# Kernel tuning notes

Hardware: AMD Instinct MI355X
Metric: run time of the kernel (lower is better)

The kernel has to match this reference:

```python
import jax, jax.numpy as jnp
import numpy as np

A = 10      # number of areas of interest
NPA = 192   # neurons per area
C = 128     # n_channels_per_region
B, T = 32, 1024
N = A * NPA # 1920 total neurons


def setup_inputs() -> dict:
    key = jax.random.key(0)
    k1, k2, k3 = jax.random.split(key, 3)
    x = jax.random.normal(k1, (B, T, N), jnp.float32)
    # per-area linear weights, stored [A, n_in, n_out] (nn.Linear W.T), and biases
    W = jax.random.normal(k2, (A, NPA, C), jnp.float32) / np.sqrt(NPA)
    b = jax.random.normal(k3, (A, C), jnp.float32) * 0.01
    # area label per neuron, identical across batch (code uses neuron_regions[0]);
    # permute neuron order so the per-area gather is irregular
    labels = jnp.repeat(jnp.arange(A, dtype=jnp.int32), NPA)
    perm = jax.random.permutation(jax.random.key(7), N)
    labels = labels[perm]
    neuron_regions = jnp.tile(labels[None, :], (B, 1))
    is_left = jnp.zeros((B, N), dtype=bool)  # unused by forward body
    return {"x": x, "W": W, "b": b, "neuron_regions": neuron_regions, "is_left": is_left}


def reference(x, W, b, neuron_regions, is_left):
    # halfbin_X=0, smoothing=False -> preprocess_X is identity, repeat_interleave no-op
    nr = np.asarray(neuron_regions[0])                      # static per-session labels
    A_, n, C_ = W.shape
    # gather indices per area; equal counts per area -> rectangular [A, n]
    idx = np.stack([np.where(nr == a)[0] for a in range(A_)])
    x_area = x[:, :, idx]                                   # [B, T, A, n] gather
    emb = jnp.einsum('btan,anc->btac', x_area, W) + b       # per-area small linear
    Bq, Tq = x.shape[0], x.shape[1]
    # scatter: area a writes channels [a*C, (a+1)*C) -> contiguous reshape
    return emb.reshape(Bq, Tq, A_ * C_)
```

## Files before the change

### kernel.cpp

```cpp
#include <hip/hip_runtime.h>
#include <stdint.h>

#define A_    10
#define NPA_  192
#define C_    128
#define N_    1920
#define M_    32768
#define OUTC  1280
#define MT    16
#define RS    1928

typedef __attribute__((ext_vector_type(8))) short  short8;
typedef __attribute__((ext_vector_type(4))) float  float4v;

__device__ __forceinline__ unsigned short f2bf(float f) {
  unsigned u = __builtin_bit_cast(unsigned, f);
  u += 0x7FFFu + ((u >> 16) & 1u);
  return (unsigned short)(u >> 16);
}

__global__ __launch_bounds__(256) void prep_kernel(const float* __restrict__ W,
                                                   const int* __restrict__ nr,
                                                   unsigned short* __restrict__ Wt,
                                                   int* __restrict__ dest) {
  if (blockIdx.x == 0) {
    int lane = threadIdx.x;
    if (lane < 64) {
      int cnt[A_];
#pragma unroll
      for (int i = 0; i < A_; ++i) cnt[i] = 0;
      unsigned long long lt = (1ull << lane) - 1ull;
      for (int ch = 0; ch < N_ / 64; ++ch) {
        int p = ch * 64 + lane;
        int a = nr[p];
        int base = 0, rank = 0;
#pragma unroll
        for (int aa = 0; aa < A_; ++aa) {
          unsigned long long m = __ballot(a == aa);
          if (a == aa) { base = cnt[aa]; rank = __popcll(m & lt); }
          cnt[aa] += __popcll(m);
        }
        dest[p] = a * NPA_ + base + rank;
      }
    }
  } else {
    int o  = (blockIdx.x - 1) * 256 + threadIdx.x;
    int ac = o / NPA_;
    int k  = o - ac * NPA_;
    int a  = ac >> 7;
    int c  = ac & 127;
    Wt[o] = f2bf(W[(a * NPA_ + k) * C_ + c]);
  }
}

__global__ __launch_bounds__(256, 2) void stitch_kernel(const float* __restrict__ x,
                                                        const unsigned short* __restrict__ Wt,
                                                        const float* __restrict__ bias,
                                                        const int* __restrict__ dest,
                                                        float* __restrict__ out) {
  __shared__ unsigned short xs[MT * RS];

  const int tid = threadIdx.x;
  const int mb  = blockIdx.x * MT;

  const float4* xp = (const float4*)(x + (size_t)mb * N_);
  const int4*   dp = (const int4*)dest;
#pragma unroll
  for (int i = 0; i < 30; ++i) {
    int g   = i * 256 + tid;
    int row = g / 480;
    int c4  = g - row * 480;
    float4 v = xp[g];
    int4   d = dp[c4];
    unsigned short* base = xs + row * RS;
    base[d.x] = f2bf(v.x);
    base[d.y] = f2bf(v.y);
    base[d.z] = f2bf(v.z);
    base[d.w] = f2bf(v.w);
  }
  __syncthreads();

  const int wave = tid >> 6;
  const int lane = tid & 63;
  const int l15  = lane & 15;
  const int lq   = lane >> 4;

  short8 af[6];
  int    cur_a = -1;
  const int t0 = wave * 20;

  short8 bf[6];
  {
    int t = t0, a = t >> 3, cc = t & 7;
    const short8* wp = (const short8*)(Wt + (size_t)(a * C_ + cc * 16 + l15) * NPA_);
#pragma unroll
    for (int ks = 0; ks < 6; ++ks) bf[ks] = wp[ks * 4 + lq];
  }

  for (int t = t0; t < t0 + 20; ++t) {
    int a = t >> 3, cc = t & 7;
    if (a != cur_a) {
#pragma unroll
      for (int ks = 0; ks < 6; ++ks)
        af[ks] = *(const short8*)&xs[l15 * RS + a * NPA_ + ks * 32 + lq * 8];
      cur_a = a;
    }
    float bv = bias[a * C_ + cc * 16 + l15];

    short8 bfn[6];
    if (t + 1 < t0 + 20) {
      int t2 = t + 1, a2 = t2 >> 3, cc2 = t2 & 7;
      const short8* wp2 = (const short8*)(Wt + (size_t)(a2 * C_ + cc2 * 16 + l15) * NPA_);
#pragma unroll
      for (int ks = 0; ks < 6; ++ks) bfn[ks] = wp2[ks * 4 + lq];
    }

    float4v acc = {0.f, 0.f, 0.f, 0.f};
#pragma unroll
    for (int ks = 0; ks < 6; ++ks)
      acc = __builtin_amdgcn_mfma_f32_16x16x32_bf16(af[ks], bf[ks], acc, 0, 0, 0);

    float* op = out + (size_t)(mb + lq * 4) * OUTC + a * C_ + cc * 16 + l15;
#pragma unroll
    for (int r = 0; r < 4; ++r) op[(size_t)r * OUTC] = acc[r] + bv;

#pragma unroll
    for (int ks = 0; ks < 6; ++ks) bf[ks] = bfn[ks];
  }
}

extern "C" void kernel_launch(void* const* d_in, const int* in_sizes, int n_in,
                              void* d_out, int out_size, void* d_ws, size_t ws_size,
                              hipStream_t stream) {
  const float* x    = (const float*)d_in[0];
  const float* W    = (const float*)d_in[1];
  const float* b    = (const float*)d_in[2];
  const int*   nr   = (const int*)  d_in[3];
  float*       out  = (float*)d_out;

  unsigned short* Wt   = (unsigned short*)d_ws;
  int*            dest = (int*)((char*)d_ws + 491520);

  prep_kernel<<<dim3(961), dim3(256), 0, stream>>>(W, nr, Wt, dest);
  stitch_kernel<<<dim3(M_ / MT), dim3(256), 0, stream>>>(x, Wt, b, dest, out);
}
```

Measured before the change: 489.0 us.

## Use 32-row tiles with 1024-thread blocks and stage dest indices in LDS

Doubles the row tile to 32 and quadruples the block to 16 waves. Each wave now computes two 16-row MFMA tiles per weight fragment, which halves weight reloads per row. The dest permutation is cached in LDS rather than reread from global memory on every scatter. The LDS footprint grows to about 131KB via dynamic shared memory, which limits occupancy to one block per CU and leaves fewer blocks (1024) to overlap load and compute.

```diff
diff --git a/kernel.cpp b/kernel.cpp
--- a/kernel.cpp
+++ b/kernel.cpp
@@ -7,8 +7,9 @@
 #define N_    1920
 #define M_    32768
 #define OUTC  1280
-#define MT    16
+#define MT    32
 #define RS    1928
+#define LDS_BYTES (MT*RS*2 + N_*4)
 
 typedef __attribute__((ext_vector_type(8))) short  short8;
 typedef __attribute__((ext_vector_type(4))) float  float4v;
@@ -53,25 +54,29 @@
   }
 }
 
-__global__ __launch_bounds__(256, 2) void stitch_kernel(const float* __restrict__ x,
-                                                        const unsigned short* __restrict__ Wt,
-                                                        const float* __restrict__ bias,
-                                                        const int* __restrict__ dest,
-                                                        float* __restrict__ out) {
-  __shared__ unsigned short xs[MT * RS];
+__global__ __launch_bounds__(1024, 4) void stitch_kernel(const float* __restrict__ x,
+                                                         const unsigned short* __restrict__ Wt,
+                                                         const float* __restrict__ bias,
+                                                         const int* __restrict__ dest,
+                                                         float* __restrict__ out) {
+  extern __shared__ char smem[];
+  unsigned short* xs   = (unsigned short*)smem;
+  int*            dlds = (int*)(smem + MT * RS * 2);
 
   const int tid = threadIdx.x;
   const int mb  = blockIdx.x * MT;
 
+  if (tid < 480) ((int4*)dlds)[tid] = ((const int4*)dest)[tid];
+  __syncthreads();
+
   const float4* xp = (const float4*)(x + (size_t)mb * N_);
-  const int4*   dp = (const int4*)dest;
 #pragma unroll
-  for (int i = 0; i < 30; ++i) {
-    int g   = i * 256 + tid;
+  for (int i = 0; i < 15; ++i) {
+    int g   = i * 1024 + tid;
     int row = g / 480;
     int c4  = g - row * 480;
     float4 v = xp[g];
-    int4   d = dp[c4];
+    int4   d = ((const int4*)dlds)[c4];
     unsigned short* base = xs + row * RS;
     base[d.x] = f2bf(v.x);
     base[d.y] = f2bf(v.y);
@@ -85,44 +90,53 @@
   const int l15  = lane & 15;
   const int lq   = lane >> 4;
 
-  short8 af[6];
+  short8 af0[6], af1[6];
   int    cur_a = -1;
-  const int t0 = wave * 20;
+  const int p0 = wave * 5;
 
   short8 bf[6];
   {
-    int t = t0, a = t >> 3, cc = t & 7;
+    int p = p0, a = p >> 3, cc = p & 7;
     const short8* wp = (const short8*)(Wt + (size_t)(a * C_ + cc * 16 + l15) * NPA_);
 #pragma unroll
     for (int ks = 0; ks < 6; ++ks) bf[ks] = wp[ks * 4 + lq];
   }
 
-  for (int t = t0; t < t0 + 20; ++t) {
-    int a = t >> 3, cc = t & 7;
+  for (int p = p0; p < p0 + 5; ++p) {
+    int a = p >> 3, cc = p & 7;
     if (a != cur_a) {
 #pragma unroll
-      for (int ks = 0; ks < 6; ++ks)
-        af[ks] = *(const short8*)&xs[l15 * RS + a * NPA_ + ks * 32 + lq * 8];
+      for (int ks = 0; ks < 6; ++ks) {
+        af0[ks] = *(const short8*)&xs[l15 * RS + a * NPA_ + ks * 32 + lq * 8];
+        af1[ks] = *(const short8*)&xs[(16 + l15) * RS + a * NPA_ + ks * 32 + lq * 8];
+      }
       cur_a = a;
     }
     float bv = bias[a * C_ + cc * 16 + l15];
 
     short8 bfn[6];
-    if (t + 1 < t0 + 20) {
-      int t2 = t + 1, a2 = t2 >> 3, cc2 = t2 & 7;
+    if (p + 1 < p0 + 5) {
+      int p2 = p + 1, a2 = p2 >> 3, cc2 = p2 & 7;
       const short8* wp2 = (const short8*)(Wt + (size_t)(a2 * C_ + cc2 * 16 + l15) * NPA_);
 #pragma unroll
       for (int ks = 0; ks < 6; ++ks) bfn[ks] = wp2[ks * 4 + lq];
     }
 
-    float4v acc = {0.f, 0.f, 0.f, 0.f};
+    float4v acc0 = {0.f, 0.f, 0.f, 0.f};
+    float4v acc1 = {0.f, 0.f, 0.f, 0.f};
 #pragma unroll
-    for (int ks = 0; ks < 6; ++ks)
-      acc = __builtin_amdgcn_mfma_f32_16x16x32_bf16(af[ks], bf[ks], acc, 0, 0, 0);
+    for (int ks = 0; ks < 6; ++ks) {
+      acc0 = __builtin_amdgcn_mfma_f32_16x16x32_bf16(af0[ks], bf[ks], acc0, 0, 0, 0);
+      acc1 = __builtin_amdgcn_mfma_f32_16x16x32_bf16(af1[ks], bf[ks], acc1, 0, 0, 0);
+    }
 
-    float* op = out + (size_t)(mb + lq * 4) * OUTC + a * C_ + cc * 16 + l15;
+    float* op0 = out + (size_t)(mb + lq * 4) * OUTC + a * C_ + cc * 16 + l15;
+    float* op1 = op0 + (size_t)16 * OUTC;
 #pragma unroll
-    for (int r = 0; r < 4; ++r) op[(size_t)r * OUTC] = acc[r] + bv;
+    for (int r = 0; r < 4; ++r) {
+      op0[(size_t)r * OUTC] = acc0[r] + bv;
+      op1[(size_t)r * OUTC] = acc1[r] + bv;
+    }
 
 #pragma unroll
     for (int ks = 0; ks < 6; ++ks) bf[ks] = bfn[ks];
@@ -141,6 +155,13 @@
   unsigned short* Wt   = (unsigned short*)d_ws;
   int*            dest = (int*)((char*)d_ws + 491520);
 
+  static int lds_attr_set = 0;
+  if (!lds_attr_set) {
+    hipFuncSetAttribute((const void*)stitch_kernel,
+                        hipFuncAttributeMaxDynamicSharedMemorySize, LDS_BYTES);
+    lds_attr_set = 1;
+  }
+
   prep_kernel<<<dim3(961), dim3(256), 0, stream>>>(W, nr, Wt, dest);
-  stitch_kernel<<<dim3(M_ / MT), dim3(256), 0, stream>>>(x, Wt, b, dest, out);
+  stitch_kernel<<<dim3(M_ / MT), dim3(1024), LDS_BYTES, stream>>>(x, Wt, b, dest, out);
 }
```

After: 452.6 us. -7.4%, faster.
